# Performance work log

Hardware: AMD Instinct MI355X
Metric: run time of the kernel (lower is better)

## Reference

```python
import jax, jax.numpy as jnp
import numpy as np

B, S, E, H = 2, 2048, 1024, 16
D = E // H


def setup_inputs() -> dict:
    key = jax.random.key(0)
    ks = jax.random.split(key, 8)
    hidden_states = jax.random.normal(ks[0], (B, S, E), dtype=jnp.float32)
    # q/k/v projections: small random init
    Wq = jax.random.normal(ks[1], (E, E), dtype=jnp.float32) * 0.02
    Wk = jax.random.normal(ks[2], (E, E), dtype=jnp.float32) * 0.02
    Wv = jax.random.normal(ks[3], (E, E), dtype=jnp.float32) * 0.02
    bq = jnp.zeros((E,), jnp.float32)
    bk = jnp.zeros((E,), jnp.float32)
    bv = jnp.zeros((E,), jnp.float32)
    # hedgehog feature maps: identity init (per init_weights_) + small noise
    eye = jnp.eye(E, dtype=jnp.float32)
    Wfq = eye + jax.random.normal(ks[4], (E, E), dtype=jnp.float32) * 0.02
    Wfk = eye + jax.random.normal(ks[5], (E, E), dtype=jnp.float32) * 0.02
    bfq = jnp.zeros((E,), jnp.float32)
    bfk = jnp.zeros((E,), jnp.float32)
    return dict(hidden_states=hidden_states, Wq=Wq, bq=bq, Wk=Wk, bk=bk,
                Wv=Wv, bv=bv, Wfq=Wfq, bfq=bfq, Wfk=Wfk, bfk=bfk)


def reference(hidden_states, Wq, bq, Wk, bk, Wv, bv, Wfq, bfq, Wfk, bfk):
    b, s, e = hidden_states.shape
    d = e // H
    # feature maps: linear -> linear -> softmax over full hidden dim (before head split)
    q = jax.nn.softmax((hidden_states @ Wq.T + bq) @ Wfq.T + bfq, axis=-1)
    k = jax.nn.softmax((hidden_states @ Wk.T + bk) @ Wfk.T + bfk, axis=-1)
    v = hidden_states @ Wv.T + bv
    split = lambda t: t.reshape(b, s, H, d).transpose(0, 2, 1, 3)  # [B,H,S,D]
    q, k, v = split(q), split(k), split(v)
    scores = jnp.einsum('bhsd,bhtd->bhst', q, k)          # [B,H,S,S], nonnegative
    probs = scores / jnp.sum(scores, axis=-1, keepdims=True)  # sum-normalization
    ctx = jnp.einsum('bhst,bhtd->bhsd', probs, v)
    return ctx.transpose(0, 2, 1, 3).reshape(b, s, e)
```

## Files before the change

kernel.cpp:

```cpp
#include <hip/hip_runtime.h>
#include <math.h>

constexpr int B = 2, S = 2048, E = 1024, H = 16, D = 64;
constexpr int M = B * S;
constexpr int NBIG = 3072;
constexpr int CH = 8;

typedef __attribute__((ext_vector_type(8))) _Float16 half8;
typedef __attribute__((ext_vector_type(8))) short short8;
typedef __attribute__((ext_vector_type(4))) float f32x4;
#define MFMA_F16 __builtin_amdgcn_mfma_f32_16x16x32_f16
#define WAITCNT_VM(N) __builtin_amdgcn_s_waitcnt(0xF70 | (N))

__device__ __forceinline__ short f2h(float f) {
  _Float16 h = (_Float16)f;
  short s;
  __builtin_memcpy(&s, &h, 2);
  return s;
}
__device__ __forceinline__ float h2f(short s) {
  _Float16 h;
  __builtin_memcpy(&h, &s, 2);
  return (float)h;
}

__device__ __forceinline__ void gload16(const void* g, const void* l) {
  __builtin_amdgcn_global_load_lds(
      (const __attribute__((address_space(1))) unsigned*)g,
      (__attribute__((address_space(3))) unsigned*)l, 16, 0, 0);
}

template <int BM>
__device__ __forceinline__ void gemm_core(const short* __restrict__ A,
                                          const short* __restrict__ Bm,
                                          int bm, int bn, int K, short* lds,
                                          f32x4 (&acc)[BM / 32][4]) {
  constexpr int SA = BM / 16, TOT = SA + 8, PW = TOT / 4, MT = BM / 32;
  const int tid = threadIdx.x, wave = tid >> 6, lane = tid & 63;

  const short* gb[PW];
#pragma unroll
  for (int j = 0; j < PW; ++j) {
    const int n = wave * PW + j;
    const short* src; int seg, rowbase;
    if (n < SA) { src = A;  seg = n;      rowbase = bm; }
    else        { src = Bm; seg = n - SA; rowbase = bn; }
    const int r = seg * 16 + (lane >> 2);
    const int p = lane & 3;
    const int q = (p - ((r >> 1) & 3)) & 3;
    gb[j] = src + (size_t)(rowbase + r) * K + q * 8;
  }
  const int fr = lane & 15, fq = lane >> 4;
  const int wm = (wave & 1) * (BM / 2), wn = (wave >> 1) * 64;
  int ao[MT], bo[4];
#pragma unroll
  for (int mi = 0; mi < MT; ++mi) {
    const int r = wm + mi * 16 + fr;
    ao[mi] = r * 32 + (((fq + ((r >> 1) & 3)) & 3)) * 8;
  }
#pragma unroll
  for (int ni = 0; ni < 4; ++ni) {
    const int r = wn + ni * 16 + fr;
    bo[ni] = BM * 32 + r * 32 + (((fq + ((r >> 1) & 3)) & 3)) * 8;
  }
  const int ldsW = wave * PW * 512;
  auto stageAll = [&](int buf, int k0) {
#pragma unroll
    for (int j = 0; j < PW; ++j)
      gload16(gb[j] + k0, &lds[buf * TOT * 512 + ldsW + j * 512]);
  };
  stageAll(0, 0);
  stageAll(1, 32);
  int buf = 0;
  for (int k0 = 0; k0 < K; k0 += 32) {
    if (k0 + 32 < K) WAITCNT_VM(PW); else WAITCNT_VM(0);
    __builtin_amdgcn_s_barrier();
    half8 ah[MT], bh4[4];
    const int bb = buf * TOT * 512;
#pragma unroll
    for (int mi = 0; mi < MT; ++mi) ah[mi] = *(const half8*)&lds[bb + ao[mi]];
#pragma unroll
    for (int ni = 0; ni < 4; ++ni) bh4[ni] = *(const half8*)&lds[bb + bo[ni]];
#pragma unroll
    for (int mi = 0; mi < MT; ++mi)
#pragma unroll
      for (int ni = 0; ni < 4; ++ni)
        acc[mi][ni] = MFMA_F16(ah[mi], bh4[ni], acc[mi][ni], 0, 0, 0);
    __builtin_amdgcn_s_barrier();
    if (k0 + 64 < K) stageAll(buf, k0 + 64);
    buf ^= 1;
  }
}

__global__ __launch_bounds__(256) void prep_w(
    const float* __restrict__ Wfq, short* Wfq_f,
    const float* __restrict__ Wfk, short* Wfk_f,
    const float* __restrict__ Wv, short* Wv_f,
    const float* __restrict__ Wq, short* WqT_f,
    const float* __restrict__ Wk, short* WkT_f,
    const float* __restrict__ bq, const float* __restrict__ bfq,
    const float* __restrict__ bk, const float* __restrict__ bfk,
    const float* __restrict__ bv, float* bcat, float* Zk) {
  __shared__ float tb[32][33];
  const int blk = blockIdx.x, tid = threadIdx.x;
  if (blk < 768) {
    const int base = blk;
    const float* src = (base < 256) ? Wfq : (base < 512 ? Wfk : Wv);
    short* dst = (base < 256) ? Wfq_f : (base < 512 ? Wfk_f : Wv_f);
    const int bb = base & 255;
#pragma unroll
    for (int p = 0; p < 4; ++p) {
      const int i = bb * 1024 + p * 256 + tid;
      float4 v = ((const float4*)src)[i];
      ((short4*)dst)[i] = make_short4(f2h(v.x), f2h(v.y), f2h(v.z), f2h(v.w));
    }
  } else if (blk < 2816) {
    const int t = blk - 768;
    const float* in = (t < 1024) ? Wq : Wk;
    short* oh = (t < 1024) ? WqT_f : WkT_f;
    const int tt = t & 1023;
    const int bx = (tt & 31) * 32, by = (tt >> 5) * 32;
    const int x = tid & 31, y0 = tid >> 5;
#pragma unroll
    for (int i = 0; i < 32; i += 8) tb[y0 + i][x] = in[(size_t)(by + y0 + i) * E + bx + x];
    __syncthreads();
#pragma unroll
    for (int i = 0; i < 32; i += 8)
      oh[(size_t)(bx + y0 + i) * E + by + x] = f2h(tb[x][y0 + i]);
  } else if (blk < 3328) {
    const int t = blk - 2816;
    const float* Wf = (t < 256) ? Wfq : Wfk;
    const float* bin = (t < 256) ? bq : bk;
    const float* bf = (t < 256) ? bfq : bfk;
    float* o = (t < 256) ? bcat : bcat + 1024;
    const int n = (t & 255) * 4 + (tid >> 6);
    const int lane = tid & 63;
    float sacc = 0.f;
    for (int j = lane; j < E; j += 64) sacc += Wf[(size_t)n * E + j] * bin[j];
#pragma unroll
    for (int off = 32; off; off >>= 1) sacc += __shfl_xor(sacc, off, 64);
    if (lane == 0) o[n] = sacc + bf[n];
  } else {
    ((float4*)(bcat + 2048))[tid] = ((const float4*)bv)[tid];
#pragma unroll
    for (int p = 0; p < 4; ++p)
      ((float4*)Zk)[p * 256 + tid] = make_float4(0.f, 0.f, 0.f, 0.f);
  }
}

__global__ __launch_bounds__(256, 3) void wgemm_hs(
    const short* __restrict__ Wfq_f, const short* __restrict__ WqT_f,
    const short* __restrict__ Wfk_f, const short* __restrict__ WkT_f,
    short* __restrict__ Wcat,
    const float* __restrict__ hs, short* __restrict__ hs_f) {
  __shared__ short lds[2 * 16 * 512];
  if (blockIdx.z == 2) {
    const int bid = blockIdx.y * 8 + blockIdx.x;
    const int stride = 64 * 256;
    for (int i = bid * 256 + threadIdx.x; i < M * E / 4; i += stride) {
      float4 v = ((const float4*)hs)[i];
      ((short4*)hs_f)[i] = make_short4(f2h(v.x), f2h(v.y), f2h(v.z), f2h(v.w));
    }
    return;
  }
  const short* A = blockIdx.z ? Wfk_f : Wfq_f;
  const short* Bm = blockIdx.z ? WkT_f : WqT_f;
  short* C = Wcat + (size_t)blockIdx.z * E * E;
  const int bm = blockIdx.x * 128, bn = blockIdx.y * 128;
  f32x4 acc[4][4] = {};
  gemm_core<128>(A, Bm, bm, bn, E, lds, acc);
  const int lane = threadIdx.x & 63, wave = threadIdx.x >> 6;
  const int fr = lane & 15, fq = lane >> 4;
  const int wm = (wave & 1) * 64, wn = (wave >> 1) * 64;
#pragma unroll
  for (int ni = 0; ni < 4; ++ni) {
    const int n = bn + wn + ni * 16 + fr;
#pragma unroll
    for (int mi = 0; mi < 4; ++mi) {
      const int m0 = bm + wm + mi * 16 + fq * 4;
#pragma unroll
      for (int r2 = 0; r2 < 4; ++r2)
        C[(size_t)(m0 + r2) * E + n] = f2h(acc[mi][ni][r2]);
    }
  }
}

__global__ __launch_bounds__(256, 3) void gemm_big(
    const short* __restrict__ hs_f, const short* __restrict__ Wcat,
    const float* __restrict__ bcat, short* __restrict__ Cb,
    float* __restrict__ Zk) {
  __shared__ short lds[2 * 16 * 512];
  const int bm = blockIdx.y * 128, bn = blockIdx.x * 128;
  f32x4 acc[4][4] = {};
  gemm_core<128>(hs_f, Wcat, bm, bn, E, lds, acc);
  const int lane = threadIdx.x & 63, wave = threadIdx.x >> 6;
  const int fr = lane & 15, fq = lane >> 4;
  const int wm = (wave & 1) * 64, wn = (wave >> 1) * 64;
  const bool doExp = (bn < 2048);
  const bool doZ = (bn >= 1024) && (bn < 2048);
  float bv4[4];
#pragma unroll
  for (int ni = 0; ni < 4; ++ni) bv4[ni] = bcat[bn + wn + ni * 16 + fr];
#pragma unroll
  for (int mi = 0; mi < 4; ++mi)
#pragma unroll
    for (int r2 = 0; r2 < 4; ++r2) {
      const int m = bm + wm + mi * 16 + fq * 4 + r2;
      float vals[4];
#pragma unroll
      for (int ni = 0; ni < 4; ++ni) vals[ni] = acc[mi][ni][r2] + bv4[ni];
      if (doExp) {
#pragma unroll
        for (int ni = 0; ni < 4; ++ni) vals[ni] = __expf(vals[ni]);
      }
      if (doZ) {
        float es = vals[0] + vals[1] + vals[2] + vals[3];
#pragma unroll
        for (int off = 1; off < 16; off <<= 1) es += __shfl_xor(es, off, 16);
        if (fr == 0) atomicAdd(&Zk[m], es);
      }
#pragma unroll
      for (int ni = 0; ni < 4; ++ni)
        Cb[(size_t)m * NBIG + bn + wn + ni * 16 + fr] = f2h(vals[ni]);
    }
}

__global__ __launch_bounds__(512) void kv_part(const short* __restrict__ Cb,
                                               const float* __restrict__ Zk,
                                               float* __restrict__ KVp,
                                               float* __restrict__ ksump) {
  const int bh = blockIdx.x;
  const int b = bh / H, h = bh % H;
  const int t0 = blockIdx.y * 256;
  const short* kbase = Cb + (size_t)b * S * NBIG + 1024 + h * D;
  const short* vbase = Cb + (size_t)b * S * NBIG + 2048 + h * D;
  __shared__ float ks[32][D];
  __shared__ float vs[32][D];
  __shared__ float invZs[256];
  __shared__ float red[20][256];
  const int tid = threadIdx.x;
  if (tid < 256) invZs[tid] = 1.0f / Zk[b * S + t0 + tid];
  const int t2 = tid & 255;
  const int g = tid >> 8;
  const int a4 = t2 & 15, b4 = t2 >> 4;
  const int lt = tid >> 4, d4 = (tid & 15) * 4;
  float acc[4][4] = {};
  float ksm[4] = {};
  for (int ts = 0; ts < 256; ts += 32) {
    __syncthreads();
    const size_t roff = (size_t)(t0 + ts + lt) * NBIG + d4;
    short4 k4 = *(const short4*)(kbase + roff);
    short4 v4 = *(const short4*)(vbase + roff);
    const float iz = invZs[ts + lt];
    ks[lt][d4 + 0] = h2f(k4.x) * iz; ks[lt][d4 + 1] = h2f(k4.y) * iz;
    ks[lt][d4 + 2] = h2f(k4.z) * iz; ks[lt][d4 + 3] = h2f(k4.w) * iz;
    vs[lt][d4 + 0] = h2f(v4.x); vs[lt][d4 + 1] = h2f(v4.y);
    vs[lt][d4 + 2] = h2f(v4.z); vs[lt][d4 + 3] = h2f(v4.w);
    __syncthreads();
    const int tb = g * 16;
#pragma unroll
    for (int tt = 0; tt < 16; ++tt) {
      const float4 kk = *(const float4*)&ks[tb + tt][a4 * 4];
      const float4 vv = *(const float4*)&vs[tb + tt][b4 * 4];
      const float kk4[4] = {kk.x, kk.y, kk.z, kk.w};
      const float vv4[4] = {vv.x, vv.y, vv.z, vv.w};
#pragma unroll
      for (int i = 0; i < 4; ++i) {
        ksm[i] += kk4[i];
#pragma unroll
        for (int j = 0; j < 4; ++j) acc[i][j] = fmaf(kk4[i], vv4[j], acc[i][j]);
      }
    }
  }
  __syncthreads();
  if (g) {
#pragma unroll
    for (int e = 0; e < 16; ++e) red[e][t2] = acc[e >> 2][e & 3];
#pragma unroll
    for (int i = 0; i < 4; ++i) red[16 + i][t2] = ksm[i];
  }
  __syncthreads();
  if (!g) {
#pragma unroll
    for (int i = 0; i < 4; ++i) {
      ksm[i] += red[16 + i][t2];
#pragma unroll
      for (int j = 0; j < 4; ++j) acc[i][j] += red[i * 4 + j][t2];
    }
    float* kvout = KVp + ((size_t)bh * CH + blockIdx.y) * 4096;
#pragma unroll
    for (int i = 0; i < 4; ++i)
      *(float4*)&kvout[(a4 * 4 + i) * 64 + b4 * 4] =
          make_float4(acc[i][0], acc[i][1], acc[i][2], acc[i][3]);
    if (b4 == 0)
      *(float4*)&ksump[((size_t)bh * CH + blockIdx.y) * 64 + a4 * 4] =
          make_float4(ksm[0], ksm[1], ksm[2], ksm[3]);
  }
}

__global__ __launch_bounds__(256) void out_v9(const short* __restrict__ Cb,
                                              const float* __restrict__ KVp,
                                              const float* __restrict__ ksump,
                                              float* __restrict__ out) {
  const int bh = blockIdx.x;
  const int b = bh >> 4, h = bh & 15;
  __shared__ float KVs[64][64];
  __shared__ float kss[64];
  __shared__ float qs_t[4][64][20];
  __shared__ float dns[64];
  const int tid = threadIdx.x, wave = tid >> 6, lane = tid & 63;
  const int g = lane & 15, rg = lane >> 4;
  const int row0 = blockIdx.y * 64;
  const int qrow = row0 + wave * 16 + g;
  const int dstart = rg * 16;
  const short* qp = Cb + (size_t)(b * S + qrow) * NBIG + h * 64 + dstart;
  const short8 u8a = *(const short8*)qp;
  const short8 u8b = *(const short8*)(qp + 8);
  for (int i = tid; i < 1024; i += 256) {
    float4 s = make_float4(0.f, 0.f, 0.f, 0.f);
#pragma unroll
    for (int c = 0; c < CH; ++c) {
      float4 p = ((const float4*)(KVp + ((size_t)bh * CH + c) * 4096))[i];
      s.x += p.x; s.y += p.y; s.z += p.z; s.w += p.w;
    }
    ((float4*)KVs)[i] = s;
  }
  if (tid < 16) {
    float4 s = make_float4(0.f, 0.f, 0.f, 0.f);
#pragma unroll
    for (int c = 0; c < CH; ++c) {
      float4 p = ((const float4*)(ksump + ((size_t)bh * CH + c) * 64))[tid];
      s.x += p.x; s.y += p.y; s.z += p.z; s.w += p.w;
    }
    ((float4*)kss)[tid] = s;
  }
  __syncthreads();
  float uf[16];
#pragma unroll
  for (int j = 0; j < 8; ++j) { uf[j] = h2f(u8a[j]); uf[8 + j] = h2f(u8b[j]); }
  float dnp = 0.f;
#pragma unroll
  for (int j = 0; j < 16; ++j) {
    qs_t[wave][dstart + j][g] = uf[j];
    dnp = fmaf(uf[j], kss[dstart + j], dnp);
  }
  dnp += __shfl_xor(dnp, 16, 64);
  dnp += __shfl_xor(dnp, 32, 64);
  if (rg == 0) dns[wave * 16 + g] = dnp;
  __syncthreads();
  float acc[4][4] = {};
#pragma unroll
  for (int d = 0; d < 64; ++d) {
    const float4 kv = *(const float4*)&KVs[d][g * 4];
    const float4 q4 = *(const float4*)&qs_t[wave][d][rg * 4];
    const float qa[4] = {q4.x, q4.y, q4.z, q4.w};
    const float ka[4] = {kv.x, kv.y, kv.z, kv.w};
#pragma unroll
    for (int i = 0; i < 4; ++i)
#pragma unroll
      for (int j = 0; j < 4; ++j) acc[i][j] = fmaf(qa[i], ka[j], acc[i][j]);
  }
#pragma unroll
  for (int i = 0; i < 4; ++i) {
    const int r = wave * 16 + rg * 4 + i;
    const float inv = 1.0f / dns[r];
    const int row = row0 + r;
    float4 o4 = make_float4(acc[i][0] * inv, acc[i][1] * inv,
                            acc[i][2] * inv, acc[i][3] * inv);
    *(float4*)(out + ((size_t)b * S + row) * E + h * 64 + g * 4) = o4;
  }
}

extern "C" void kernel_launch(void* const* d_in, const int* in_sizes, int n_in,
                              void* d_out, int out_size, void* d_ws, size_t ws_size,
                              hipStream_t stream) {
  const float* hs = (const float*)d_in[0];
  const float* Wq = (const float*)d_in[1];
  const float* bq = (const float*)d_in[2];
  const float* Wk = (const float*)d_in[3];
  const float* bk = (const float*)d_in[4];
  const float* Wv = (const float*)d_in[5];
  const float* bv = (const float*)d_in[6];
  const float* Wfq = (const float*)d_in[7];
  const float* bfq = (const float*)d_in[8];
  const float* Wfk = (const float*)d_in[9];
  const float* bfk = (const float*)d_in[10];
  float* out = (float*)d_out;

  const size_t MEG = 1024 * 1024;
  float* ws = (float*)d_ws;
  short* hs_f = (short*)ws;
  short* Wfq_f = (short*)(ws + 2 * MEG);
  short* Wfk_f = (short*)(ws + 2 * MEG + MEG / 2);
  short* WqT_f = (short*)(ws + 3 * MEG);
  short* WkT_f = (short*)(ws + 3 * MEG + MEG / 2);
  short* Wcat = (short*)(ws + 4 * MEG);
  short* Wv_f = Wcat + 2 * MEG;
  float* bcat = ws + 6 * MEG;
  float* Zk = bcat + 4096;
  float* KVp = ws + 7 * MEG;
  float* ksump = ws + 8 * MEG;
  short* Cbig = (short*)(ws + 9 * MEG);

  prep_w<<<3329, 256, 0, stream>>>(Wfq, Wfq_f, Wfk, Wfk_f, Wv, Wv_f,
                                   Wq, WqT_f, Wk, WkT_f,
                                   bq, bfq, bk, bfk, bv, bcat, Zk);
  wgemm_hs<<<dim3(8, 8, 3), 256, 0, stream>>>(Wfq_f, WqT_f, Wfk_f, WkT_f,
                                              Wcat, hs, hs_f);
  gemm_big<<<dim3(24, 32), 256, 0, stream>>>(hs_f, Wcat, bcat, Cbig, Zk);
  kv_part<<<dim3(B * H, CH), 512, 0, stream>>>(Cbig, Zk, KVp, ksump);
  out_v9<<<dim3(B * H, S / 64), 256, 0, stream>>>(Cbig, KVp, ksump, out);
}
```

Baseline: 180.3 us.

## Replace big projection GEMM with 256x256 tile, 8-wave pipelined kernel

The main fused projection GEMM moves from a 128x128 tile with 4 waves to a 256x256 tile with 8 waves. It uses a 128KB double-buffered LDS with XOR swizzling and splits each k-step into four MFMA phases, interleaving half-tile global loads with compute and raising MFMA priority. The aim is more operand reuse per LDS load and better overlap of loads with MFMA. The cost is a grid of only 192 blocks, which may underfill the 256 CUs, plus many barriers and heavy register pressure.

Result: no change. 183.9 us (+2.0%).

```diff
diff --git a/kernel.cpp b/kernel.cpp
--- a/kernel.cpp
+++ b/kernel.cpp
@@ -5,6 +5,7 @@
 constexpr int M = B * S;
 constexpr int NBIG = 3072;
 constexpr int CH = 8;
+constexpr int NT = 16;
 
 typedef __attribute__((ext_vector_type(8))) _Float16 half8;
 typedef __attribute__((ext_vector_type(8))) short short8;
@@ -185,27 +186,111 @@
   }
 }
 
-__global__ __launch_bounds__(256, 3) void gemm_big(
-    const short* __restrict__ hs_f, const short* __restrict__ Wcat,
+#define LOAD_A(MH)                                                           \
+  _Pragma("unroll") for (int mq = 0; mq < 4; ++mq)                           \
+  _Pragma("unroll") for (int ks = 0; ks < 2; ++ks)                           \
+      a[mq][ks] = *(const half8*)&lds[pb + (MH)*8192 + aoff[mq][ks]];
+#define LOAD_B(NH)                                                           \
+  _Pragma("unroll") for (int nq = 0; nq < 2; ++nq)                           \
+  _Pragma("unroll") for (int ks = 0; ks < 2; ++ks)                           \
+      b[nq][ks] = *(const half8*)&lds[pb + 16384 + (NH)*8192 + boff[nq][ks]];
+#define PHASE_MFMA(MB, NB)                                                   \
+  __builtin_amdgcn_s_setprio(1);                                             \
+  _Pragma("unroll") for (int ks = 0; ks < 2; ++ks)                           \
+  _Pragma("unroll") for (int mq = 0; mq < 4; ++mq)                           \
+  _Pragma("unroll") for (int nq = 0; nq < 2; ++nq)                           \
+      acc[(MB) + mq][(NB) + nq] =                                            \
+          MFMA_F16(a[mq][ks], b[nq][ks], acc[(MB) + mq][(NB) + nq], 0, 0, 0);\
+  __builtin_amdgcn_s_setprio(0);
+
+__global__ __launch_bounds__(512, 2) void gemm_big8(
+    const short* __restrict__ A, const short* __restrict__ Bm,
     const float* __restrict__ bcat, short* __restrict__ Cb,
     float* __restrict__ Zk) {
-  __shared__ short lds[2 * 16 * 512];
-  const int bm = blockIdx.y * 128, bn = blockIdx.x * 128;
-  f32x4 acc[4][4] = {};
-  gemm_core<128>(hs_f, Wcat, bm, bn, E, lds, acc);
-  const int lane = threadIdx.x & 63, wave = threadIdx.x >> 6;
+  __shared__ __align__(16) short lds[65536];
+  const int tid = threadIdx.x, wave = tid >> 6, lane = tid & 63;
   const int fr = lane & 15, fq = lane >> 4;
-  const int wm = (wave & 1) * 64, wn = (wave >> 1) * 64;
+  const int wm = wave >> 2, wnq = wave & 3;
+  const int bm = blockIdx.y * 256, bn = blockIdx.x * 256;
+
+  const int srow = lane >> 3;
+  const int xk = ((lane & 7) ^ srow) * 8;
+
+  auto stage_half = [&](int th, int ty) {
+    if (th >= NT) return;
+    const int p = (th & 1) * 32768;
+    const short* src; int rowBase, slot;
+    if (ty == 0)      { src = A;  rowBase = bm;       slot = p; }
+    else if (ty == 1) { src = Bm; rowBase = bn + 128; slot = p + 24576; }
+    else if (ty == 2) { src = A;  rowBase = bm + 128; slot = p + 8192; }
+    else              { src = Bm; rowBase = bn;       slot = p + 16384; }
+    const int k0 = th * 64 + xk;
+#pragma unroll
+    for (int j = 0; j < 2; ++j)
+      gload16(src + (size_t)(rowBase + (wave * 2 + j) * 8 + srow) * 1024 + k0,
+              &lds[slot + (wave * 2 + j) * 512]);
+  };
+
+  int aoff[4][2], boff[2][2];
+#pragma unroll
+  for (int mq = 0; mq < 4; ++mq)
+#pragma unroll
+    for (int ks = 0; ks < 2; ++ks)
+      aoff[mq][ks] = (wm * 64 + mq * 16 + fr) * 64 +
+                     ((ks * 32 + fq * 8) ^ ((fr & 7) << 3));
+#pragma unroll
+  for (int nq = 0; nq < 2; ++nq)
+#pragma unroll
+    for (int ks = 0; ks < 2; ++ks)
+      boff[nq][ks] = (wnq * 32 + nq * 16 + fr) * 64 +
+                     ((ks * 32 + fq * 8) ^ ((fr & 7) << 3));
+
+  f32x4 acc[8][4] = {};
+  half8 a[4][2], b[2][2];
+
+  stage_half(0, 0); stage_half(0, 1); stage_half(0, 2); stage_half(0, 3);
+  stage_half(1, 0); stage_half(1, 1); stage_half(1, 2);
+
+  for (int u = 0; u < NT; ++u) {
+    const int pb = (u & 1) * 32768;
+    stage_half(u + 1, 3);
+    if (u < NT - 1) { WAITCNT_VM(6); } else { WAITCNT_VM(0); }
+    __builtin_amdgcn_s_barrier();
+    LOAD_A(0);
+    LOAD_B(0);
+    PHASE_MFMA(0, 0);
+    __builtin_amdgcn_s_barrier();
+    LOAD_B(1);
+    stage_half(u + 2, 0);
+    __builtin_amdgcn_s_barrier();
+    PHASE_MFMA(0, 2);
+    __builtin_amdgcn_s_barrier();
+    LOAD_A(1);
+    stage_half(u + 2, 1);
+    __builtin_amdgcn_s_barrier();
+    PHASE_MFMA(4, 2);
+    __builtin_amdgcn_s_barrier();
+    LOAD_B(0);
+    stage_half(u + 2, 2);
+    __builtin_amdgcn_s_barrier();
+    PHASE_MFMA(4, 0);
+    __builtin_amdgcn_s_barrier();
+  }
+
   const bool doExp = (bn < 2048);
   const bool doZ = (bn >= 1024) && (bn < 2048);
   float bv4[4];
-#pragma unroll
-  for (int ni = 0; ni < 4; ++ni) bv4[ni] = bcat[bn + wn + ni * 16 + fr];
-#pragma unroll
-  for (int mi = 0; mi < 4; ++mi)
+  int ncol[4];
+#pragma unroll
+  for (int ni = 0; ni < 4; ++ni) {
+    ncol[ni] = bn + (ni >> 1) * 128 + wnq * 32 + (ni & 1) * 16 + fr;
+    bv4[ni] = bcat[ncol[ni]];
+  }
+#pragma unroll
+  for (int mi = 0; mi < 8; ++mi)
 #pragma unroll
     for (int r2 = 0; r2 < 4; ++r2) {
-      const int m = bm + wm + mi * 16 + fq * 4 + r2;
+      const int m = bm + (mi >> 2) * 128 + wm * 64 + (mi & 3) * 16 + fq * 4 + r2;
       float vals[4];
 #pragma unroll
       for (int ni = 0; ni < 4; ++ni) vals[ni] = acc[mi][ni][r2] + bv4[ni];
@@ -221,7 +306,7 @@
       }
 #pragma unroll
       for (int ni = 0; ni < 4; ++ni)
-        Cb[(size_t)m * NBIG + bn + wn + ni * 16 + fr] = f2h(vals[ni]);
+        Cb[(size_t)m * NBIG + ncol[ni]] = f2h(vals[ni]);
     }
 }
 
@@ -407,7 +492,7 @@
                                    bq, bfq, bk, bfk, bv, bcat, Zk);
   wgemm_hs<<<dim3(8, 8, 3), 256, 0, stream>>>(Wfq_f, WqT_f, Wfk_f, WkT_f,
                                               Wcat, hs, hs_f);
-  gemm_big<<<dim3(24, 32), 256, 0, stream>>>(hs_f, Wcat, bcat, Cbig, Zk);
+  gemm_big8<<<dim3(12, 16), 512, 0, stream>>>(hs_f, Wcat, bcat, Cbig, Zk);
   kv_part<<<dim3(B * H, CH), 512, 0, stream>>>(Cbig, Zk, KVp, ksump);
   out_v9<<<dim3(B * H, S / 64), 256, 0, stream>>>(Cbig, KVp, ksump, out);
 }
```
